# Optimization experiments

Measured on AMD Instinct MI355X. Metric: run time of the kernel, lower is better.

The kernel has to match this reference:

```python
import jax, jax.numpy as jnp
import numpy as np

D_MODEL = 1024
NHEAD = 16
HEAD_DIM = D_MODEL // NHEAD


def setup_inputs() -> dict:
    key = jax.random.key(0)
    ks = jax.random.split(key, 9)
    s = 0.02
    x = jax.random.normal(ks[0], (2, 2048, D_MODEL), dtype=jnp.float32)
    Wq = jax.random.normal(ks[1], (D_MODEL, D_MODEL), dtype=jnp.float32) * s
    bq = jnp.zeros((D_MODEL,), jnp.float32)
    Wk = jax.random.normal(ks[2], (D_MODEL, D_MODEL), dtype=jnp.float32) * s
    bk = jnp.zeros((D_MODEL,), jnp.float32)
    Wv = jax.random.normal(ks[3], (D_MODEL, D_MODEL), dtype=jnp.float32) * s
    bv = jnp.zeros((D_MODEL,), jnp.float32)
    Wo = jax.random.normal(ks[4], (D_MODEL, D_MODEL), dtype=jnp.float32) * s
    bo = jnp.zeros((D_MODEL,), jnp.float32)
    return {"x": x, "Wq": Wq, "bq": bq, "Wk": Wk, "bk": bk,
            "Wv": Wv, "bv": bv, "Wo": Wo, "bo": bo}


def _rope(x, sin, cos):
    # x: [B, L, H, Dh]; rotate-half as in the torch module
    half = x.shape[-1] // 2
    x1, x2 = x[..., :half], x[..., half:]
    rotated = jnp.concatenate([-x2, x1], axis=-1)
    return x * cos + rotated * sin


def reference(x, Wq, bq, Wk, bk, Wv, bv, Wo, bo):
    B, L, D = x.shape
    H, Dh = NHEAD, HEAD_DIM
    q = (x @ Wq.T + bq).reshape(B, L, H, Dh)
    k = (x @ Wk.T + bk).reshape(B, L, H, Dh)
    v = (x @ Wv.T + bv).reshape(B, L, H, Dh)

    inv_freq = 1.0 / (10000.0 ** (jnp.arange(0, Dh, 2, dtype=jnp.float32) / Dh))
    t = jnp.arange(L, dtype=jnp.float32)
    freqs = jnp.einsum('i,j->ij', t, inv_freq)          # [L, Dh/2]
    emb = jnp.concatenate([freqs, freqs], axis=-1)      # [L, Dh]
    cos = jnp.cos(emb)[None, :, None, :]
    sin = jnp.sin(emb)[None, :, None, :]

    q = _rope(q, sin, cos)
    k = _rope(k, sin, cos)

    # [B, H, L, L]
    scores = jnp.einsum('bqhd,bkhd->bhqk', q, k) / jnp.sqrt(jnp.float32(Dh))
    attn = jax.nn.softmax(scores, axis=-1)
    # dropout in eval mode = identity (p given as 0.0)
    out = jnp.einsum('bhqk,bkhd->bqhd', attn, v).reshape(B, L, D)
    return out @ Wo.T + bo
```

## Files before the change

### kernel.cpp

```cpp
#include <hip/hip_runtime.h>
#include <math.h>

#define D_MODEL 1024
#define NHEAD 16
#define HEAD_DIM 64
#define L_SEQ 2048
#define BATCH 2
#define M_ROWS 4096
#define SC_Q 0.18033688011112042f

typedef __attribute__((ext_vector_type(8))) short short8;
typedef __attribute__((ext_vector_type(4))) float floatx4;
typedef __attribute__((ext_vector_type(2))) __fp16 half2_t;
typedef __attribute__((ext_vector_type(4))) __fp16 half4_t;

#if __has_builtin(__builtin_amdgcn_exp2f)
#define EXP2F(x) __builtin_amdgcn_exp2f(x)
#else
#define EXP2F(x) exp2f(x)
#endif

__device__ inline unsigned f2bf_u(float x) {
    unsigned u = __float_as_uint(x);
    return (u + 0x7fffu + ((u >> 16) & 1u)) >> 16;
}

__device__ inline void gl_lds16(const void* g, void* l) {
    __builtin_amdgcn_global_load_lds((const __attribute__((address_space(1))) void*)g,
                                     (__attribute__((address_space(3))) void*)l, 16, 0, 0);
}

__global__ __launch_bounds__(256) void cvt_all(
    const float* __restrict__ x,  const float* __restrict__ wq,
    const float* __restrict__ wk, const float* __restrict__ wv,
    const float* __restrict__ wo,
    unsigned short* __restrict__ xb,  unsigned short* __restrict__ wqb,
    unsigned short* __restrict__ wkb, unsigned short* __restrict__ wvb,
    unsigned short* __restrict__ wob, float* __restrict__ rt) {
    if (blockIdx.y == 5) {
        for (int idx = blockIdx.x * 256 + threadIdx.x; idx < L_SEQ * 16;
             idx += gridDim.x * 256) {
            int l = idx >> 4, f = idx & 15;
            float if0 = (float)pow(10000.0, -(double)f / 32.0);
            float if1 = (float)pow(10000.0, -(double)(f + 16) / 32.0);
            float s0, c0, s1, c1;
            sincosf((float)l * if0, &s0, &c0);
            sincosf((float)l * if1, &s1, &c1);
            float4 v = {c0, c1, s0, s1};
            *(float4*)(rt + (size_t)idx * 4) = v;
        }
        return;
    }
    const float* s; unsigned short* d; int n;
    switch (blockIdx.y) {
        case 0:  s = x;  d = xb;  n = M_ROWS * D_MODEL; break;
        case 1:  s = wq; d = wqb; n = D_MODEL * D_MODEL; break;
        case 2:  s = wk; d = wkb; n = D_MODEL * D_MODEL; break;
        case 3:  s = wv; d = wvb; n = D_MODEL * D_MODEL; break;
        default: s = wo; d = wob; n = D_MODEL * D_MODEL; break;
    }
    int stride = gridDim.x * 256 * 4;
    for (int i = (blockIdx.x * 256 + threadIdx.x) * 4; i < n; i += stride) {
        float4 v = *(const float4*)(s + i);
        ushort4 o;
        o.x = (unsigned short)f2bf_u(v.x);
        o.y = (unsigned short)f2bf_u(v.y);
        o.z = (unsigned short)f2bf_u(v.z);
        o.w = (unsigned short)f2bf_u(v.w);
        *(ushort4*)(d + i) = o;
    }
}

__global__ __launch_bounds__(256) void gemm_qkv(
    const unsigned short* __restrict__ xb,
    const unsigned short* __restrict__ wqb, const unsigned short* __restrict__ wkb,
    const unsigned short* __restrict__ wvb,
    const float* __restrict__ bq, const float* __restrict__ bk,
    const float* __restrict__ bv, const float* __restrict__ rt,
    unsigned short* __restrict__ qo, unsigned short* __restrict__ ko,
    unsigned short* __restrict__ vo) {
    __shared__ __align__(16) unsigned short As[128 * 32];
    __shared__ __align__(16) unsigned short Bs[128 * 32];

    const int K = D_MODEL;
    const int tid = threadIdx.x;
    const int lane = tid & 63;
    const int w = tid >> 6;
    const int wm = (w & 1) * 64;
    const int wn = (w >> 1) * 64;
    const int m0 = blockIdx.x * 128;
    const int n0 = blockIdx.y * 128;

    const unsigned short* Wsel; const float* bsel;
    unsigned short* osel; int mode; float oscale;
    if (blockIdx.z == 0)      { Wsel = wqb; bsel = bq; osel = qo; mode = 1; oscale = SC_Q; }
    else if (blockIdx.z == 1) { Wsel = wkb; bsel = bk; osel = ko; mode = 1; oscale = 1.0f; }
    else                      { Wsel = wvb; bsel = bv; osel = vo; mode = 2; oscale = 1.0f; }

    floatx4 acc[4][4];
#pragma unroll
    for (int i = 0; i < 4; ++i)
#pragma unroll
        for (int j = 0; j < 4; ++j) acc[i][j] = (floatx4){0.f, 0.f, 0.f, 0.f};

    const int sr = lane >> 2;
    const int ss = lane & 3;
    const unsigned short* Ag = xb + (size_t)m0 * K;
    const unsigned short* Bg = Wsel + (size_t)n0 * K;

    for (int k0 = 0; k0 < K; k0 += 32) {
        __syncthreads();
#pragma unroll
        for (int t = 0; t < 2; ++t) {
            int R0 = t * 64 + w * 16;
            int r = R0 + sr;
            int c = ss ^ ((r >> 1) & 3);
            gl_lds16(Ag + (size_t)r * K + k0 + c * 8, (void*)(As + R0 * 32));
            gl_lds16(Bg + (size_t)r * K + k0 + c * 8, (void*)(Bs + R0 * 32));
        }
        __syncthreads();

        short8 af[4], bf[4];
#pragma unroll
        for (int mt = 0; mt < 4; ++mt) {
            int ar = wm + mt * 16 + (lane & 15);
            int slot = (lane >> 4) ^ ((ar >> 1) & 3);
            af[mt] = *(const short8*)(As + ar * 32 + slot * 8);
        }
#pragma unroll
        for (int nt = 0; nt < 4; ++nt) {
            int br = wn + nt * 16 + (lane & 15);
            int slot = (lane >> 4) ^ ((br >> 1) & 3);
            bf[nt] = *(const short8*)(Bs + br * 32 + slot * 8);
        }
#pragma unroll
        for (int mt = 0; mt < 4; ++mt)
#pragma unroll
            for (int nt = 0; nt < 4; ++nt)
                acc[mt][nt] = __builtin_amdgcn_mfma_f32_16x16x32_bf16(
                    af[mt], bf[nt], acc[mt][nt], 0, 0, 0);
    }

#pragma unroll
    for (int nt = 0; nt < 4; ++nt) {
        float bn = bsel[n0 + wn + nt * 16 + (lane & 15)];
#pragma unroll
        for (int mt = 0; mt < 4; ++mt)
#pragma unroll
            for (int i = 0; i < 4; ++i) acc[mt][nt][i] += bn;
    }

    const int h = (n0 + wn) >> 6;

    if (mode == 1) {
#pragma unroll
        for (int mt = 0; mt < 4; ++mt)
#pragma unroll
            for (int i = 0; i < 4; ++i) {
                int m = m0 + wm + mt * 16 + (lane >> 4) * 4 + i;
                int b = m >> 11, l = m & (L_SEQ - 1);
                float4 tc = *(const float4*)(rt + ((size_t)(l * 16 + (lane & 15)) << 2));
#pragma unroll
                for (int nt = 0; nt < 4; ++nt) {
                    int dh = nt * 16 + (lane & 15);
                    float partner = acc[mt][nt ^ 2][i];
                    float rot = (nt < 2) ? -partner : partner;
                    float c = (nt & 1) ? tc.y : tc.x;
                    float s = (nt & 1) ? tc.w : tc.z;
                    float val = (acc[mt][nt][i] * c + rot * s) * oscale;
                    size_t idx = (((size_t)(b * NHEAD + h)) * L_SEQ + l) * HEAD_DIM + dh;
                    osel[idx] = (unsigned short)f2bf_u(val);
                }
            }
    } else {
#pragma unroll
        for (int mt = 0; mt < 4; ++mt)
#pragma unroll
            for (int ih = 0; ih < 4; ih += 2) {
                int m = m0 + wm + mt * 16 + (lane >> 4) * 4 + ih;
                int b = m >> 11, l = m & (L_SEQ - 1);
#pragma unroll
                for (int nt = 0; nt < 4; ++nt) {
                    int dh = nt * 16 + (lane & 15);
                    union { half2_t h; unsigned u; } cv;
                    cv.h = __builtin_amdgcn_cvt_pkrtz(acc[mt][nt][ih], acc[mt][nt][ih + 1]);
                    size_t idx = (((size_t)(b * NHEAD + h)) * HEAD_DIM + dh) * L_SEQ + l;
                    *(unsigned*)(vo + idx) = cv.u;
                }
            }
    }
}

__global__ __launch_bounds__(256) void gemm_out(
    const unsigned short* __restrict__ A, const unsigned short* __restrict__ Wb,
    const float* __restrict__ bias, float* __restrict__ out) {
    __shared__ __align__(16) unsigned short As[64 * 32];
    __shared__ __align__(16) unsigned short Bs[128 * 32];

    const int K = D_MODEL;
    const int tid = threadIdx.x;
    const int lane = tid & 63;
    const int w = tid >> 6;
    const int wm = (w & 1) * 32;
    const int wn = (w >> 1) * 64;
    const int m0 = blockIdx.x * 64;
    const int n0 = blockIdx.y * 128;

    floatx4 acc[2][4];
#pragma unroll
    for (int i = 0; i < 2; ++i)
#pragma unroll
        for (int j = 0; j < 4; ++j) acc[i][j] = (floatx4){0.f, 0.f, 0.f, 0.f};

    const int sr = lane >> 2;
    const int ss = lane & 3;
    const unsigned short* Ag = A + (size_t)m0 * K;
    const unsigned short* Bg = Wb + (size_t)n0 * K;

    for (int k0 = 0; k0 < K; k0 += 32) {
        __syncthreads();
        {
            int r = w * 16 + sr;
            int c = ss ^ ((r >> 1) & 3);
            gl_lds16(Ag + (size_t)r * K + k0 + c * 8, (void*)(As + (w * 16) * 32));
        }
#pragma unroll
        for (int t = 0; t < 2; ++t) {
            int R0 = t * 64 + w * 16;
            int r = R0 + sr;
            int c = ss ^ ((r >> 1) & 3);
            gl_lds16(Bg + (size_t)r * K + k0 + c * 8, (void*)(Bs + R0 * 32));
        }
        __syncthreads();

        short8 af[2], bf[4];
#pragma unroll
        for (int mt = 0; mt < 2; ++mt) {
            int ar = wm + mt * 16 + (lane & 15);
            int slot = (lane >> 4) ^ ((ar >> 1) & 3);
            af[mt] = *(const short8*)(As + ar * 32 + slot * 8);
        }
#pragma unroll
        for (int nt = 0; nt < 4; ++nt) {
            int br = wn + nt * 16 + (lane & 15);
            int slot = (lane >> 4) ^ ((br >> 1) & 3);
            bf[nt] = *(const short8*)(Bs + br * 32 + slot * 8);
        }
#pragma unroll
        for (int mt = 0; mt < 2; ++mt)
#pragma unroll
            for (int nt = 0; nt < 4; ++nt)
                acc[mt][nt] = __builtin_amdgcn_mfma_f32_16x16x32_bf16(
                    af[mt], bf[nt], acc[mt][nt], 0, 0, 0);
    }

#pragma unroll
    for (int nt = 0; nt < 4; ++nt) {
        int n = n0 + wn + nt * 16 + (lane & 15);
        float bn = bias[n];
#pragma unroll
        for (int mt = 0; mt < 2; ++mt)
#pragma unroll
            for (int i = 0; i < 4; ++i) {
                int m = m0 + wm + mt * 16 + (lane >> 4) * 4 + i;
                out[(size_t)m * D_MODEL + n] = acc[mt][nt][i] + bn;
            }
    }
}

template <int NZ>
__global__ __launch_bounds__(256, 4) void attn_mfma(
    const unsigned short* __restrict__ q, const unsigned short* __restrict__ k,
    const unsigned short* __restrict__ vt,
    float* __restrict__ opart, float* __restrict__ lpart,
    unsigned short* __restrict__ ao) {
    __shared__ __align__(16) unsigned short Ks[128 * 64];
    __shared__ __align__(16) unsigned short Vs[64 * 128];

    const int tid = threadIdx.x;
    const int lane = tid & 63;
    const int w = tid >> 6;
    const int quad = lane >> 4;
    const int ln = lane & 15;
    const int bh = blockIdx.y;
    const int q0 = blockIdx.x * 128;
    const int z = blockIdx.z;
    const int kvbase = z * (L_SEQ / NZ);

    const unsigned short* qb = q + (size_t)bh * L_SEQ * HEAD_DIM;
    const unsigned short* kb = k + (size_t)bh * L_SEQ * HEAD_DIM;
    const unsigned short* vb = vt + (size_t)bh * HEAD_DIM * L_SEQ;

    short8 qf[2][2];
#pragma unroll
    for (int ntq = 0; ntq < 2; ++ntq)
#pragma unroll
        for (int ks = 0; ks < 2; ++ks)
            qf[ntq][ks] = *(const short8*)(
                qb + (size_t)(q0 + w * 32 + ntq * 16 + ln) * HEAD_DIM
                + ks * 32 + quad * 8);

    floatx4 o[2][4];
    floatx4 ls[2];
#pragma unroll
    for (int ntq = 0; ntq < 2; ++ntq) {
        ls[ntq] = (floatx4){0.f, 0.f, 0.f, 0.f};
#pragma unroll
        for (int j = 0; j < 4; ++j) o[ntq][j] = (floatx4){0.f, 0.f, 0.f, 0.f};
    }

    half4_t ones;
#pragma unroll
    for (int j = 0; j < 4; ++j) ones[j] = (__fp16)1.0f;

    const int srk = lane >> 3;
    const int ssk = lane & 7;
    const int srv = lane >> 4;
    const int ssv = lane & 15;

    for (int t = 0; t < L_SEQ / (128 * NZ); ++t) {
        int kv0 = kvbase + t * 128;
        __syncthreads();
#pragma unroll
        for (int tt = 0; tt < 4; ++tt) {
            {
                int R0 = tt * 32 + w * 8;
                int r = R0 + srk;
                int c = ssk ^ (r & 7);
                gl_lds16(kb + (size_t)(kv0 + r) * HEAD_DIM + c * 8, (void*)(Ks + R0 * 64));
            }
            {
                int R0 = tt * 16 + w * 4;
                int r = R0 + srv;
                int c = ssv ^ (r & 15);
                gl_lds16(vb + (size_t)r * L_SEQ + kv0 + c * 8, (void*)(Vs + R0 * 128));
            }
        }
        __syncthreads();

#pragma unroll
        for (int mt = 0; mt < 8; ++mt) {
            int ar = mt * 16 + ln;
            short8 kf0 = *(const short8*)(Ks + ar * 64 + ((quad) ^ (ar & 7)) * 8);
            short8 kf1 = *(const short8*)(Ks + ar * 64 + ((4 + quad) ^ (ar & 7)) * 8);

            floatx4 s0 = (floatx4){0.f, 0.f, 0.f, 0.f};
            floatx4 s1 = (floatx4){0.f, 0.f, 0.f, 0.f};
            s0 = __builtin_amdgcn_mfma_f32_16x16x32_bf16(kf0, qf[0][0], s0, 0, 0, 0);
            s0 = __builtin_amdgcn_mfma_f32_16x16x32_bf16(kf1, qf[0][1], s0, 0, 0, 0);
            s1 = __builtin_amdgcn_mfma_f32_16x16x32_bf16(kf0, qf[1][0], s1, 0, 0, 0);
            s1 = __builtin_amdgcn_mfma_f32_16x16x32_bf16(kf1, qf[1][1], s1, 0, 0, 0);

            half4_t vf[4];
#pragma unroll
            for (int ntd = 0; ntd < 4; ++ntd) {
                int row = ntd * 16 + ln;
                int slot = (mt * 2 + (quad >> 1)) ^ ln;
                vf[ntd] = *(const half4_t*)(Vs + row * 128 + slot * 8 + (quad & 1) * 4);
            }

            {
                half2_t lo = __builtin_amdgcn_cvt_pkrtz(EXP2F(s0[0]), EXP2F(s0[1]));
                half2_t hi = __builtin_amdgcn_cvt_pkrtz(EXP2F(s0[2]), EXP2F(s0[3]));
                half4_t af; af.lo = lo; af.hi = hi;
                ls[0] = __builtin_amdgcn_mfma_f32_16x16x16f16(af, ones, ls[0], 0, 0, 0);
#pragma unroll
                for (int ntd = 0; ntd < 4; ++ntd)
                    o[0][ntd] = __builtin_amdgcn_mfma_f32_16x16x16f16(af, vf[ntd], o[0][ntd], 0, 0, 0);
            }
            {
                half2_t lo = __builtin_amdgcn_cvt_pkrtz(EXP2F(s1[0]), EXP2F(s1[1]));
                half2_t hi = __builtin_amdgcn_cvt_pkrtz(EXP2F(s1[2]), EXP2F(s1[3]));
                half4_t af; af.lo = lo; af.hi = hi;
                ls[1] = __builtin_amdgcn_mfma_f32_16x16x16f16(af, ones, ls[1], 0, 0, 0);
#pragma unroll
                for (int ntd = 0; ntd < 4; ++ntd)
                    o[1][ntd] = __builtin_amdgcn_mfma_f32_16x16x16f16(af, vf[ntd], o[1][ntd], 0, 0, 0);
            }
        }
    }

    if (NZ == 1) {
        const int b = bh >> 4, h = bh & (NHEAD - 1);
#pragma unroll
        for (int ntq = 0; ntq < 2; ++ntq)
#pragma unroll
            for (int i = 0; i < 4; ++i) {
                int l = q0 + w * 32 + ntq * 16 + quad * 4 + i;
                float inv = 1.0f / ls[ntq][i];
#pragma unroll
                for (int ntd = 0; ntd < 4; ++ntd) {
                    int dh = ntd * 16 + ln;
                    size_t idx = ((size_t)b * L_SEQ + l) * D_MODEL + h * HEAD_DIM + dh;
                    ao[idx] = (unsigned short)f2bf_u(o[ntq][ntd][i] * inv);
                }
            }
    } else {
        const size_t base = ((size_t)z * (BATCH * NHEAD) + bh) * L_SEQ;
#pragma unroll
        for (int ntq = 0; ntq < 2; ++ntq)
#pragma unroll
            for (int i = 0; i < 4; ++i) {
                int l = q0 + w * 32 + ntq * 16 + quad * 4 + i;
#pragma unroll
                for (int ntd = 0; ntd < 4; ++ntd) {
                    int dh = ntd * 16 + ln;
                    opart[(base + l) * HEAD_DIM + dh] = o[ntq][ntd][i];
                }
            }
        if (ln == 0) {
#pragma unroll
            for (int ntq = 0; ntq < 2; ++ntq)
#pragma unroll
                for (int i = 0; i < 4; ++i) {
                    int l = q0 + w * 32 + ntq * 16 + quad * 4 + i;
                    lpart[base + l] = ls[ntq][i];
                }
        }
    }
}

__global__ __launch_bounds__(256) void attn_combine(
    const float* __restrict__ opart, const float* __restrict__ lpart,
    unsigned short* __restrict__ ao) {
    const size_t R = (size_t)BATCH * NHEAD * L_SEQ;
    int e = blockIdx.x * 256 + threadIdx.x;
    int r = e >> 4;
    int dh0 = (e & 15) * 4;
    float4 a = *(const float4*)(opart + (size_t)r * HEAD_DIM + dh0);
    float4 c = *(const float4*)(opart + (R + r) * HEAD_DIM + dh0);
    float inv = 1.0f / (lpart[r] + lpart[R + r]);
    int bh = r >> 11, l = r & (L_SEQ - 1);
    int b = bh >> 4, h = bh & (NHEAD - 1);
    ushort4 ov;
    ov.x = (unsigned short)f2bf_u((a.x + c.x) * inv);
    ov.y = (unsigned short)f2bf_u((a.y + c.y) * inv);
    ov.z = (unsigned short)f2bf_u((a.z + c.z) * inv);
    ov.w = (unsigned short)f2bf_u((a.w + c.w) * inv);
    *(ushort4*)(ao + ((size_t)b * L_SEQ + l) * D_MODEL + h * HEAD_DIM + dh0) = ov;
}

extern "C" void kernel_launch(void* const* d_in, const int* in_sizes, int n_in,
                              void* d_out, int out_size, void* d_ws, size_t ws_size,
                              hipStream_t stream) {
    const float* x  = (const float*)d_in[0];
    const float* Wq = (const float*)d_in[1];
    const float* bq = (const float*)d_in[2];
    const float* Wk = (const float*)d_in[3];
    const float* bk = (const float*)d_in[4];
    const float* Wv = (const float*)d_in[5];
    const float* bv = (const float*)d_in[6];
    const float* Wo = (const float*)d_in[7];
    const float* bo = (const float*)d_in[8];
    float* outp = (float*)d_out;

    const size_t XE = (size_t)M_ROWS * D_MODEL;
    const size_t WE = (size_t)D_MODEL * D_MODEL;
    unsigned short* wqb = (unsigned short*)d_ws;
    unsigned short* wkb = wqb + WE;
    unsigned short* wvb = wkb + WE;
    unsigned short* wob = wvb + WE;
    unsigned short* qbf = wob + WE;
    unsigned short* kbf = qbf + XE;
    unsigned short* vtb = kbf + XE;
    unsigned short* xb  = vtb + XE;
    unsigned short* aob = xb;
    float* rt    = (float*)(xb + XE);
    float* lpart = rt;
    float* opart = rt + 131072;

    const size_t base_bytes  = (4 * WE + 4 * XE) * 2 + 131072 * 4;
    const size_t split_bytes = base_bytes + (size_t)8 * 1024 * 1024 * 4;
    const bool use_split = ws_size >= split_bytes;

    cvt_all<<<dim3(1024, 6), 256, 0, stream>>>(x, Wq, Wk, Wv, Wo,
                                               xb, wqb, wkb, wvb, wob, rt);

    gemm_qkv<<<dim3(M_ROWS / 128, D_MODEL / 128, 3), 256, 0, stream>>>(
        xb, wqb, wkb, wvb, bq, bk, bv, rt, qbf, kbf, vtb);

    if (use_split) {
        attn_mfma<2><<<dim3(L_SEQ / 128, BATCH * NHEAD, 2), 256, 0, stream>>>(
            qbf, kbf, vtb, opart, lpart, nullptr);
        attn_combine<<<dim3(4096), 256, 0, stream>>>(opart, lpart, aob);
    } else {
        attn_mfma<1><<<dim3(L_SEQ / 128, BATCH * NHEAD, 1), 256, 0, stream>>>(
            qbf, kbf, vtb, nullptr, nullptr, aob);
    }

    gemm_out<<<dim3(M_ROWS / 64, D_MODEL / 128), 256, 0, stream>>>(aob, wob, bo, outp);
}
```

Baseline: 194.0 us.

## Enlarge attention query tile to 256 and use 16x16x32 f16 MFMA for PV

Each attention block now covers 256 query rows (64 per wave), so every K/V tile loaded into LDS is reused by twice as many queries. The PV product and row-sum now use the 16x16x32 f16 MFMA over 32 keys at a time. To support this, the QKV GEMM writes V^T with a permuted sequence order that matches the new fragment layout. The cost is higher register use (launch bounds drop to 2 blocks per CU) and half as many blocks in the grid.

```diff
diff --git a/kernel.cpp b/kernel.cpp
--- a/kernel.cpp
+++ b/kernel.cpp
@@ -13,6 +13,7 @@
 typedef __attribute__((ext_vector_type(4))) float floatx4;
 typedef __attribute__((ext_vector_type(2))) __fp16 half2_t;
 typedef __attribute__((ext_vector_type(4))) __fp16 half4_t;
+typedef __attribute__((ext_vector_type(8))) __fp16 half8_t;
 
 #if __has_builtin(__builtin_amdgcn_exp2f)
 #define EXP2F(x) __builtin_amdgcn_exp2f(x)
@@ -179,12 +180,14 @@
             for (int ih = 0; ih < 4; ih += 2) {
                 int m = m0 + wm + mt * 16 + (lane >> 4) * 4 + ih;
                 int b = m >> 11, l = m & (L_SEQ - 1);
+                int np = ((l >> 2) & 3) * 8 + (l & 3) + ((l >> 4) & 1) * 4;
+                int lp = (l & ~31) | np;
 #pragma unroll
                 for (int nt = 0; nt < 4; ++nt) {
                     int dh = nt * 16 + (lane & 15);
                     union { half2_t h; unsigned u; } cv;
                     cv.h = __builtin_amdgcn_cvt_pkrtz(acc[mt][nt][ih], acc[mt][nt][ih + 1]);
-                    size_t idx = (((size_t)(b * NHEAD + h)) * HEAD_DIM + dh) * L_SEQ + l;
+                    size_t idx = (((size_t)(b * NHEAD + h)) * HEAD_DIM + dh) * L_SEQ + lp;
                     *(unsigned*)(vo + idx) = cv.u;
                 }
             }
@@ -269,7 +272,7 @@
 }
 
 template <int NZ>
-__global__ __launch_bounds__(256, 4) void attn_mfma(
+__global__ __launch_bounds__(256, 2) void attn_mfma(
     const unsigned short* __restrict__ q, const unsigned short* __restrict__ k,
     const unsigned short* __restrict__ vt,
     float* __restrict__ opart, float* __restrict__ lpart,
@@ -283,7 +286,7 @@
     const int quad = lane >> 4;
     const int ln = lane & 15;
     const int bh = blockIdx.y;
-    const int q0 = blockIdx.x * 128;
+    const int q0 = blockIdx.x * 256;
     const int z = blockIdx.z;
     const int kvbase = z * (L_SEQ / NZ);
 
@@ -291,27 +294,27 @@
     const unsigned short* kb = k + (size_t)bh * L_SEQ * HEAD_DIM;
     const unsigned short* vb = vt + (size_t)bh * HEAD_DIM * L_SEQ;
 
-    short8 qf[2][2];
-#pragma unroll
-    for (int ntq = 0; ntq < 2; ++ntq)
+    short8 qf[4][2];
+#pragma unroll
+    for (int ntq = 0; ntq < 4; ++ntq)
 #pragma unroll
         for (int ks = 0; ks < 2; ++ks)
             qf[ntq][ks] = *(const short8*)(
-                qb + (size_t)(q0 + w * 32 + ntq * 16 + ln) * HEAD_DIM
+                qb + (size_t)(q0 + w * 64 + ntq * 16 + ln) * HEAD_DIM
                 + ks * 32 + quad * 8);
 
-    floatx4 o[2][4];
-    floatx4 ls[2];
-#pragma unroll
-    for (int ntq = 0; ntq < 2; ++ntq) {
-        ls[ntq] = (floatx4){0.f, 0.f, 0.f, 0.f};
+    floatx4 o[4][4];
+    floatx4 ls4[4];
+#pragma unroll
+    for (int ntq = 0; ntq < 4; ++ntq) {
+        ls4[ntq] = (floatx4){0.f, 0.f, 0.f, 0.f};
 #pragma unroll
         for (int j = 0; j < 4; ++j) o[ntq][j] = (floatx4){0.f, 0.f, 0.f, 0.f};
     }
 
-    half4_t ones;
-#pragma unroll
-    for (int j = 0; j < 4; ++j) ones[j] = (__fp16)1.0f;
+    half8_t ones8;
+#pragma unroll
+    for (int j = 0; j < 8; ++j) ones8[j] = (__fp16)1.0f;
 
     const int srk = lane >> 3;
     const int ssk = lane & 7;
@@ -339,43 +342,44 @@
         __syncthreads();
 
 #pragma unroll
-        for (int mt = 0; mt < 8; ++mt) {
-            int ar = mt * 16 + ln;
-            short8 kf0 = *(const short8*)(Ks + ar * 64 + ((quad) ^ (ar & 7)) * 8);
-            short8 kf1 = *(const short8*)(Ks + ar * 64 + ((4 + quad) ^ (ar & 7)) * 8);
-
-            floatx4 s0 = (floatx4){0.f, 0.f, 0.f, 0.f};
-            floatx4 s1 = (floatx4){0.f, 0.f, 0.f, 0.f};
-            s0 = __builtin_amdgcn_mfma_f32_16x16x32_bf16(kf0, qf[0][0], s0, 0, 0, 0);
-            s0 = __builtin_amdgcn_mfma_f32_16x16x32_bf16(kf1, qf[0][1], s0, 0, 0, 0);
-            s1 = __builtin_amdgcn_mfma_f32_16x16x32_bf16(kf0, qf[1][0], s1, 0, 0, 0);
-            s1 = __builtin_amdgcn_mfma_f32_16x16x32_bf16(kf1, qf[1][1], s1, 0, 0, 0);
-
-            half4_t vf[4];
+        for (int pp = 0; pp < 4; ++pp) {
+            int arA = pp * 32 + ln;
+            int arB = arA + 16;
+            short8 kfA0 = *(const short8*)(Ks + arA * 64 + ((quad) ^ (arA & 7)) * 8);
+            short8 kfA1 = *(const short8*)(Ks + arA * 64 + ((4 + quad) ^ (arA & 7)) * 8);
+            short8 kfB0 = *(const short8*)(Ks + arB * 64 + ((quad) ^ (arB & 7)) * 8);
+            short8 kfB1 = *(const short8*)(Ks + arB * 64 + ((4 + quad) ^ (arB & 7)) * 8);
+
+            floatx4 sA[4], sB[4];
+#pragma unroll
+            for (int ntq = 0; ntq < 4; ++ntq) {
+                sA[ntq] = (floatx4){0.f, 0.f, 0.f, 0.f};
+                sB[ntq] = (floatx4){0.f, 0.f, 0.f, 0.f};
+                sA[ntq] = __builtin_amdgcn_mfma_f32_16x16x32_bf16(kfA0, qf[ntq][0], sA[ntq], 0, 0, 0);
+                sA[ntq] = __builtin_amdgcn_mfma_f32_16x16x32_bf16(kfA1, qf[ntq][1], sA[ntq], 0, 0, 0);
+                sB[ntq] = __builtin_amdgcn_mfma_f32_16x16x32_bf16(kfB0, qf[ntq][0], sB[ntq], 0, 0, 0);
+                sB[ntq] = __builtin_amdgcn_mfma_f32_16x16x32_bf16(kfB1, qf[ntq][1], sB[ntq], 0, 0, 0);
+            }
+
+            half8_t vf[4];
 #pragma unroll
             for (int ntd = 0; ntd < 4; ++ntd) {
                 int row = ntd * 16 + ln;
-                int slot = (mt * 2 + (quad >> 1)) ^ ln;
-                vf[ntd] = *(const half4_t*)(Vs + row * 128 + slot * 8 + (quad & 1) * 4);
-            }
-
-            {
-                half2_t lo = __builtin_amdgcn_cvt_pkrtz(EXP2F(s0[0]), EXP2F(s0[1]));
-                half2_t hi = __builtin_amdgcn_cvt_pkrtz(EXP2F(s0[2]), EXP2F(s0[3]));
-                half4_t af; af.lo = lo; af.hi = hi;
-                ls[0] = __builtin_amdgcn_mfma_f32_16x16x16f16(af, ones, ls[0], 0, 0, 0);
+                int slot = (pp * 4 + quad) ^ (row & 15);
+                vf[ntd] = *(const half8_t*)(Vs + row * 128 + slot * 8);
+            }
+
+#pragma unroll
+            for (int ntq = 0; ntq < 4; ++ntq) {
+                union { half8_t v; half2_t h[4]; } af;
+                af.h[0] = __builtin_amdgcn_cvt_pkrtz(EXP2F(sA[ntq][0]), EXP2F(sA[ntq][1]));
+                af.h[1] = __builtin_amdgcn_cvt_pkrtz(EXP2F(sA[ntq][2]), EXP2F(sA[ntq][3]));
+                af.h[2] = __builtin_amdgcn_cvt_pkrtz(EXP2F(sB[ntq][0]), EXP2F(sB[ntq][1]));
+                af.h[3] = __builtin_amdgcn_cvt_pkrtz(EXP2F(sB[ntq][2]), EXP2F(sB[ntq][3]));
+                ls4[ntq] = __builtin_amdgcn_mfma_f32_16x16x32_f16(af.v, ones8, ls4[ntq], 0, 0, 0);
 #pragma unroll
                 for (int ntd = 0; ntd < 4; ++ntd)
-                    o[0][ntd] = __builtin_amdgcn_mfma_f32_16x16x16f16(af, vf[ntd], o[0][ntd], 0, 0, 0);
-            }
-            {
-                half2_t lo = __builtin_amdgcn_cvt_pkrtz(EXP2F(s1[0]), EXP2F(s1[1]));
-                half2_t hi = __builtin_amdgcn_cvt_pkrtz(EXP2F(s1[2]), EXP2F(s1[3]));
-                half4_t af; af.lo = lo; af.hi = hi;
-                ls[1] = __builtin_amdgcn_mfma_f32_16x16x16f16(af, ones, ls[1], 0, 0, 0);
-#pragma unroll
-                for (int ntd = 0; ntd < 4; ++ntd)
-                    o[1][ntd] = __builtin_amdgcn_mfma_f32_16x16x16f16(af, vf[ntd], o[1][ntd], 0, 0, 0);
+                    o[ntq][ntd] = __builtin_amdgcn_mfma_f32_16x16x32_f16(af.v, vf[ntd], o[ntq][ntd], 0, 0, 0);
             }
         }
     }
@@ -383,11 +387,11 @@
     if (NZ == 1) {
         const int b = bh >> 4, h = bh & (NHEAD - 1);
 #pragma unroll
-        for (int ntq = 0; ntq < 2; ++ntq)
+        for (int ntq = 0; ntq < 4; ++ntq)
 #pragma unroll
             for (int i = 0; i < 4; ++i) {
-                int l = q0 + w * 32 + ntq * 16 + quad * 4 + i;
-                float inv = 1.0f / ls[ntq][i];
+                int l = q0 + w * 64 + ntq * 16 + quad * 4 + i;
+                float inv = 1.0f / ls4[ntq][i];
 #pragma unroll
                 for (int ntd = 0; ntd < 4; ++ntd) {
                     int dh = ntd * 16 + ln;
@@ -398,10 +402,10 @@
     } else {
         const size_t base = ((size_t)z * (BATCH * NHEAD) + bh) * L_SEQ;
 #pragma unroll
-        for (int ntq = 0; ntq < 2; ++ntq)
+        for (int ntq = 0; ntq < 4; ++ntq)
 #pragma unroll
             for (int i = 0; i < 4; ++i) {
-                int l = q0 + w * 32 + ntq * 16 + quad * 4 + i;
+                int l = q0 + w * 64 + ntq * 16 + quad * 4 + i;
 #pragma unroll
                 for (int ntd = 0; ntd < 4; ++ntd) {
                     int dh = ntd * 16 + ln;
@@ -410,11 +414,11 @@
             }
         if (ln == 0) {
 #pragma unroll
-            for (int ntq = 0; ntq < 2; ++ntq)
+            for (int ntq = 0; ntq < 4; ++ntq)
 #pragma unroll
                 for (int i = 0; i < 4; ++i) {
-                    int l = q0 + w * 32 + ntq * 16 + quad * 4 + i;
-                    lpart[base + l] = ls[ntq][i];
+                    int l = q0 + w * 64 + ntq * 16 + quad * 4 + i;
+                    lpart[base + l] = ls4[ntq][i];
                 }
         }
     }
@@ -480,11 +484,11 @@
         xb, wqb, wkb, wvb, bq, bk, bv, rt, qbf, kbf, vtb);
 
     if (use_split) {
-        attn_mfma<2><<<dim3(L_SEQ / 128, BATCH * NHEAD, 2), 256, 0, stream>>>(
+        attn_mfma<2><<<dim3(L_SEQ / 256, BATCH * NHEAD, 2), 256, 0, stream>>>(
             qbf, kbf, vtb, opart, lpart, nullptr);
         attn_combine<<<dim3(4096), 256, 0, stream>>>(opart, lpart, aob);
     } else {
-        attn_mfma<1><<<dim3(L_SEQ / 128, BATCH * NHEAD, 1), 256, 0, stream>>>(
+        attn_mfma<1><<<dim3(L_SEQ / 256, BATCH * NHEAD, 1), 256, 0, stream>>>(
             qbf, kbf, vtb, nullptr, nullptr, aob);
     }
 
```

Result: slower. 200.0 us (+3.1%).
